# Kernel optimization log

Hardware: AMD Instinct MI355X
Metric: run time of the kernel (lower is better)

The kernel has to match this reference:

```python
import jax, jax.numpy as jnp
import numpy as np

N, E, B = 50000, 300000, 8
XD, ED, H, L, G = 160, 16, 256, 4, 32


def setup_inputs() -> dict:
    key = jax.random.key(0)
    ks = jax.random.split(key, 24)
    w = lambda k, shape: jax.random.normal(k, shape, jnp.float32) * 0.05
    z = lambda *shape: jnp.zeros(shape, jnp.float32)
    in_dim = G + (XD - 128)
    return {
        "x": jax.random.normal(ks[0], (N, XD), jnp.float32),
        "edge_attr": jax.random.normal(ks[1], (E, ED), jnp.float32),
        "geo_w": w(ks[2], (128, G)), "geo_b": z(G),
        "nin_w1": w(ks[3], (in_dim, H)), "nin_b1": z(H),
        "nin_w2": w(ks[4], (H, H)), "nin_b2": z(H),
        "ee_w1": w(ks[5], (ED, H)), "ee_b1": z(H),
        "ee_w2": w(ks[6], (H, H)), "ee_b2": z(H),
        "msgx_w": w(ks[7], (L, H, H)),
        "msge_w": w(ks[8], (L, H, H)),
        "upd_w1": w(ks[9], (L, H, H)), "upd_b1": z(L, H),
        "upd_w2": w(ks[10], (L, H, H)), "upd_b2": z(L, H),
        "ln_g": jnp.ones((L, H), jnp.float32), "ln_b": z(L, H),
        "edge_index": jax.random.randint(ks[11], (2, E), 0, N),
        "batch": jnp.sort(jax.random.randint(ks[12], (N,), 0, B)),
        "node_type": jax.random.randint(ks[13], (N,), 0, 3),
    }


def _layernorm(v, g, b, eps=1e-5):
    mu = v.mean(-1, keepdims=True)
    var = ((v - mu) ** 2).mean(-1, keepdims=True)
    return (v - mu) / jnp.sqrt(var + eps) * g + b


def reference(x, edge_attr, geo_w, geo_b, nin_w1, nin_b1, nin_w2, nin_b2,
              ee_w1, ee_b1, ee_w2, ee_b2, msgx_w, msge_w,
              upd_w1, upd_b1, upd_w2, upd_b2, ln_g, ln_b,
              edge_index, batch, node_type):
    # geo projection of leading 128 dims, concat with remaining features
    geo = jax.nn.relu(x[:, :128] @ geo_w + geo_b)
    xin = jnp.concatenate([geo, x[:, 128:]], axis=1)
    # node_in MLP
    h = jax.nn.relu(xin @ nin_w1 + nin_b1) @ nin_w2 + nin_b2  # [N, H]
    # edge encoder MLP
    e = jax.nn.relu(edge_attr @ ee_w1 + ee_b1) @ ee_w2 + ee_b2  # [E, H]
    src, dst = edge_index[0], edge_index[1]
    for l in range(L):
        # message: msg_x(x_j) + msg_e(e), scatter-add to target nodes
        m = h[src] @ msgx_w[l] + e @ msge_w[l]  # [E, H]
        agg = jax.ops.segment_sum(m, dst, num_segments=N)  # [N, H]
        u = jax.nn.relu(agg @ upd_w1[l] + upd_b1[l]) @ upd_w2[l] + upd_b2[l]
        h = _layernorm(h + u, ln_g[l], ln_b[l])
    # masked mean-pool per graph for each node type
    def pool(k):
        mask = (node_type == k).astype(h.dtype)[:, None]  # [N, 1]
        s = jax.ops.segment_sum(h * mask, batch, num_segments=B)
        c = jax.ops.segment_sum(mask, batch, num_segments=B)
        return s / jnp.maximum(c, 1.0)
    z = jnp.concatenate([pool(0), pool(1), pool(2)], axis=1)  # [B, 3H]
    return (z, h, batch)
```

## Files before the change

kernel.cpp:

```cpp
#include <hip/hip_runtime.h>

constexpr int N  = 50000;
constexpr int E  = 300000;
constexpr int B  = 8;
constexpr int XD = 160;
constexpr int ED = 16;
constexpr int H  = 256;
constexpr int L  = 4;
constexpr int G  = 32;

typedef __attribute__((ext_vector_type(8))) short short8;
typedef __attribute__((ext_vector_type(4))) short sv4;
typedef __attribute__((ext_vector_type(4))) float floatx4;

__device__ __forceinline__ short f2bf(float f) {
    union { float f; unsigned u; } v; v.f = f;
    unsigned r = (v.u + 0x7fffu + ((v.u >> 16) & 1u)) >> 16;
    return (short)r;
}
__device__ __forceinline__ float bf2f(short s) {
    union { unsigned u; float f; } v;
    v.u = ((unsigned)(unsigned short)s) << 16;
    return v.f;
}

__global__ __launch_bounds__(256) void hist_kernel(
    const int* __restrict__ dst, int* __restrict__ cnt)
{
    int e = blockIdx.x * 256 + threadIdx.x;
    if (e < E) atomicAdd(&cnt[dst[e]], 1);
}

__global__ __launch_bounds__(256) void scan_partial_kernel(
    const int* __restrict__ cnt, int* __restrict__ bsum)
{
    __shared__ int s[256];
    const int tid = threadIdx.x;
    int i = blockIdx.x * 256 + tid;
    s[tid] = (i < N) ? cnt[i] : 0;
    __syncthreads();
    #pragma unroll
    for (int off = 128; off > 0; off >>= 1) {
        if (tid < off) s[tid] += s[tid + off];
        __syncthreads();
    }
    if (tid == 0) bsum[blockIdx.x] = s[0];
}

__global__ __launch_bounds__(256) void scan_bsum_kernel(
    int* __restrict__ bsum, int nb, int* __restrict__ rsN)
{
    __shared__ int s[256];
    const int tid = threadIdx.x;
    int v = (tid < nb) ? bsum[tid] : 0;
    s[tid] = v;
    __syncthreads();
    #pragma unroll
    for (int off = 1; off < 256; off <<= 1) {
        int x = (tid >= off) ? s[tid - off] : 0;
        __syncthreads();
        s[tid] += x;
        __syncthreads();
    }
    if (tid < nb) bsum[tid] = s[tid] - v;
    if (tid == 255) *rsN = s[255];
}

__global__ __launch_bounds__(256) void scan_final_kernel(
    const int* __restrict__ cnt, const int* __restrict__ bsum,
    int* __restrict__ rs, int* __restrict__ cursor)
{
    __shared__ int s[256];
    const int tid = threadIdx.x;
    int i = blockIdx.x * 256 + tid;
    int v = (i < N) ? cnt[i] : 0;
    s[tid] = v;
    __syncthreads();
    #pragma unroll
    for (int off = 1; off < 256; off <<= 1) {
        int x = (tid >= off) ? s[tid - off] : 0;
        __syncthreads();
        s[tid] += x;
        __syncthreads();
    }
    int excl = s[tid] - v + bsum[blockIdx.x];
    if (i < N) { rs[i] = excl; cursor[i] = excl; }
}

__global__ __launch_bounds__(256) void fill_kernel(
    const int* __restrict__ src, const int* __restrict__ dst,
    int* __restrict__ cursor, int* __restrict__ csr_src, int* __restrict__ csr_eid)
{
    int e = blockIdx.x * 256 + threadIdx.x;
    if (e < E) {
        int d = dst[e];
        int pos = atomicAdd(&cursor[d], 1);
        csr_src[pos] = src[e];
        csr_eid[pos] = e;
    }
}

__global__ __launch_bounds__(256) void hidden_agg_kernel(
    const float* __restrict__ ea, const float* __restrict__ ew1,
    const float* __restrict__ eb1,
    const int* __restrict__ rs, const int* __restrict__ csr_eid,
    short* __restrict__ haggB)
{
    const int tid = threadIdx.x;
    const int lane = tid & 63, wave = tid >> 6;
    const int n0 = blockIdx.x * 16;

    float4 w[ED];
    #pragma unroll
    for (int k = 0; k < ED; ++k)
        w[k] = *(const float4*)&ew1[k * H + 4 * lane];
    float4 bb = *(const float4*)&eb1[4 * lane];

    #pragma unroll
    for (int t = 0; t < 4; ++t) {
        int n = n0 + wave * 4 + t;
        if (n >= N) continue;
        int s = rs[n], e = rs[n + 1];
        float4 acc = {0.f, 0.f, 0.f, 0.f};
        int j = s;
        for (; j + 1 < e; j += 2) {
            int e0 = csr_eid[j], e1 = csr_eid[j + 1];
            const float* a0 = ea + (size_t)e0 * ED;
            const float* a1 = ea + (size_t)e1 * ED;
            float4 h0 = bb, h1 = bb;
            #pragma unroll
            for (int k = 0; k < ED; ++k) {
                float v0 = a0[k], v1 = a1[k];
                h0.x += v0 * w[k].x; h1.x += v1 * w[k].x;
                h0.y += v0 * w[k].y; h1.y += v1 * w[k].y;
                h0.z += v0 * w[k].z; h1.z += v1 * w[k].z;
                h0.w += v0 * w[k].w; h1.w += v1 * w[k].w;
            }
            acc.x += fmaxf(h0.x, 0.f) + fmaxf(h1.x, 0.f);
            acc.y += fmaxf(h0.y, 0.f) + fmaxf(h1.y, 0.f);
            acc.z += fmaxf(h0.z, 0.f) + fmaxf(h1.z, 0.f);
            acc.w += fmaxf(h0.w, 0.f) + fmaxf(h1.w, 0.f);
        }
        if (j < e) {
            int e0 = csr_eid[j];
            const float* a0 = ea + (size_t)e0 * ED;
            float4 h0 = bb;
            #pragma unroll
            for (int k = 0; k < ED; ++k) {
                float v0 = a0[k];
                h0.x += v0 * w[k].x; h0.y += v0 * w[k].y;
                h0.z += v0 * w[k].z; h0.w += v0 * w[k].w;
            }
            acc.x += fmaxf(h0.x, 0.f); acc.y += fmaxf(h0.y, 0.f);
            acc.z += fmaxf(h0.z, 0.f); acc.w += fmaxf(h0.w, 0.f);
        }
        sv4 o = {f2bf(acc.x), f2bf(acc.y), f2bf(acc.z), f2bf(acc.w)};
        *(sv4*)&haggB[(size_t)n * H + 4 * lane] = o;
    }
}

__global__ __launch_bounds__(256) void gather_kernel(
    const short* __restrict__ h_in_bf,
    const int* __restrict__ rs, const int* __restrict__ csr_src,
    short* __restrict__ agg_bf)
{
    const int lane = threadIdx.x & 63;
    const int wave = threadIdx.x >> 6;
    const int n = blockIdx.x * 4 + wave;
    if (n >= N) return;
    const int s = rs[n], e = rs[n + 1];
    float4 acc = {0.f, 0.f, 0.f, 0.f};
    int j = s;
    for (; j + 4 <= e; j += 4) {
        const int s0 = csr_src[j],     s1 = csr_src[j + 1];
        const int s2 = csr_src[j + 2], s3 = csr_src[j + 3];
        sv4 v0 = *(const sv4*)&h_in_bf[(size_t)s0 * H + 4 * lane];
        sv4 v1 = *(const sv4*)&h_in_bf[(size_t)s1 * H + 4 * lane];
        sv4 v2 = *(const sv4*)&h_in_bf[(size_t)s2 * H + 4 * lane];
        sv4 v3 = *(const sv4*)&h_in_bf[(size_t)s3 * H + 4 * lane];
        acc.x += (bf2f(v0.x) + bf2f(v1.x)) + (bf2f(v2.x) + bf2f(v3.x));
        acc.y += (bf2f(v0.y) + bf2f(v1.y)) + (bf2f(v2.y) + bf2f(v3.y));
        acc.z += (bf2f(v0.z) + bf2f(v1.z)) + (bf2f(v2.z) + bf2f(v3.z));
        acc.w += (bf2f(v0.w) + bf2f(v1.w)) + (bf2f(v2.w) + bf2f(v3.w));
    }
    for (; j < e; ++j) {
        const int s0 = csr_src[j];
        sv4 v0 = *(const sv4*)&h_in_bf[(size_t)s0 * H + 4 * lane];
        acc.x += bf2f(v0.x); acc.y += bf2f(v0.y);
        acc.z += bf2f(v0.z); acc.w += bf2f(v0.w);
    }
    sv4 o = {f2bf(acc.x), f2bf(acc.y), f2bf(acc.z), f2bf(acc.w)};
    *(sv4*)&agg_bf[(size_t)n * H + 4 * lane] = o;
}

__global__ __launch_bounds__(256) void wx_part_kernel(
    const float* __restrict__ msgx_w, short* __restrict__ wxwe)
{
    int l = blockIdx.x >> 8, k = blockIdx.x & 255, n = threadIdx.x;
    wxwe[((size_t)(l * H + n)) * 512 + k] = f2bf(msgx_w[((size_t)l * H + k) * H + n]);
}

__global__ __launch_bounds__(256) void we_fuse_kernel(
    const float* __restrict__ ee_w2, const float* __restrict__ msge_w,
    short* __restrict__ wxwe)
{
    __shared__ float wrow[H];
    const int tid = threadIdx.x;
    const int l = blockIdx.x / H;
    const int t = blockIdx.x % H;
    wrow[tid] = ee_w2[t * H + tid];
    __syncthreads();
    const float* mw = msge_w + (size_t)l * H * H;
    float acc = 0.f;
    for (int k = 0; k < H; ++k)
        acc += wrow[k] * mw[k * H + tid];
    wxwe[((size_t)(l * H + tid)) * 512 + 256 + t] = f2bf(acc);
}

__global__ __launch_bounds__(256) void fuse_b_kernel(
    const float* __restrict__ ee_b2, const float* __restrict__ msge_w,
    float* __restrict__ be2)
{
    __shared__ float brow[H];
    const int tid = threadIdx.x;
    const int l = blockIdx.x;
    brow[tid] = ee_b2[tid];
    __syncthreads();
    const float* mw = msge_w + (size_t)l * H * H;
    float acc = 0.f;
    for (int k = 0; k < H; ++k)
        acc += brow[k] * mw[k * H + tid];
    be2[l * H + tid] = acc;
}

__global__ __launch_bounds__(256) void conv_bt_kernel(
    const float* __restrict__ w, short* __restrict__ bt)
{
    int mat = blockIdx.x >> 8, k = blockIdx.x & 255, n = threadIdx.x;
    bt[((size_t)mat * H + n) * H + k] = f2bf(w[((size_t)mat * H + k) * H + n]);
}

__global__ __launch_bounds__(256) void geow_bt_kernel(
    const float* __restrict__ w, short* __restrict__ bt)
{
    for (int i = threadIdx.x; i < 32 * 128; i += 256) {
        int n = i >> 7, k = i & 127;
        bt[i] = f2bf(w[k * 32 + n]);
    }
}

__global__ __launch_bounds__(256) void ninw1_bt_kernel(
    const float* __restrict__ w, short* __restrict__ bt)
{
    int i = blockIdx.x * 256 + threadIdx.x;
    int n = i >> 6, k = i & 63;
    bt[i] = f2bf(w[k * H + n]);
}

__global__ __launch_bounds__(256) void node_in_mfma_kernel(
    const float* __restrict__ x,
    const short* __restrict__ geo_wbt, const float* __restrict__ geo_b,
    const short* __restrict__ w1bt, const float* __restrict__ b1,
    const short* __restrict__ w2bt, const float* __restrict__ b2,
    short* __restrict__ h_bf)
{
    constexpr int KP = H + 8;
    constexpr int KX = 128 + 8;
    constexpr int KI = 64 + 8;
    __shared__ short A[64 * KP];
    __shared__ short XIN[64 * KI];
    const int tid = threadIdx.x;
    const int lane = tid & 63, wave = tid >> 6;
    const int quad = lane >> 4, lm = lane & 15;
    const int n0 = blockIdx.x * 64;
    const int nvalid = min(64, N - n0);
    const int ncol = wave * 64 + lm;

    for (int i = tid; i < 64 * 128; i += 256) {
        int row = i >> 7, k = i & 127;
        float v = (row < nvalid) ? x[(size_t)(n0 + row) * XD + k] : 0.f;
        A[row * KX + k] = f2bf(v);
    }
    for (int i = tid; i < 64 * 32; i += 256) {
        int row = i >> 5, k = i & 31;
        float v = (row < nvalid) ? x[(size_t)(n0 + row) * XD + 128 + k] : 0.f;
        XIN[row * KI + 32 + k] = f2bf(v);
    }
    __syncthreads();

    {
        floatx4 c[2];
        float b0 = geo_b[lm], b1v = geo_b[16 + lm];
        c[0] = {b0, b0, b0, b0};
        c[1] = {b1v, b1v, b1v, b1v};
        #pragma unroll
        for (int ks = 0; ks < 4; ++ks) {
            short8 a  = *(const short8*)&A[(wave * 16 + lm) * KX + ks * 32 + quad * 8];
            short8 w0 = *(const short8*)&geo_wbt[(size_t)lm * 128 + ks * 32 + quad * 8];
            short8 w1 = *(const short8*)&geo_wbt[(size_t)(16 + lm) * 128 + ks * 32 + quad * 8];
            c[0] = __builtin_amdgcn_mfma_f32_16x16x32_bf16(a, w0, c[0], 0, 0, 0);
            c[1] = __builtin_amdgcn_mfma_f32_16x16x32_bf16(a, w1, c[1], 0, 0, 0);
        }
        #pragma unroll
        for (int nt = 0; nt < 2; ++nt)
            #pragma unroll
            for (int r = 0; r < 4; ++r) {
                int row = wave * 16 + quad * 4 + r;
                XIN[row * KI + nt * 16 + lm] = f2bf(fmaxf(c[nt][r], 0.f));
            }
    }
    __syncthreads();

    floatx4 c1[4][4];
    #pragma unroll
    for (int nt = 0; nt < 4; ++nt) {
        float bb = b1[ncol + nt * 16];
        #pragma unroll
        for (int mt = 0; mt < 4; ++mt) {
            c1[mt][nt][0] = bb; c1[mt][nt][1] = bb;
            c1[mt][nt][2] = bb; c1[mt][nt][3] = bb;
        }
    }
    #pragma unroll
    for (int ks = 0; ks < 2; ++ks) {
        short8 a[4], b[4];
        #pragma unroll
        for (int mt = 0; mt < 4; ++mt)
            a[mt] = *(const short8*)&XIN[(mt * 16 + lm) * KI + ks * 32 + quad * 8];
        #pragma unroll
        for (int nt = 0; nt < 4; ++nt)
            b[nt] = *(const short8*)&w1bt[(size_t)(ncol + nt * 16) * 64 + ks * 32 + quad * 8];
        #pragma unroll
        for (int mt = 0; mt < 4; ++mt)
            #pragma unroll
            for (int nt = 0; nt < 4; ++nt)
                c1[mt][nt] = __builtin_amdgcn_mfma_f32_16x16x32_bf16(a[mt], b[nt], c1[mt][nt], 0, 0, 0);
    }
    __syncthreads();
    #pragma unroll
    for (int mt = 0; mt < 4; ++mt)
        #pragma unroll
        for (int nt = 0; nt < 4; ++nt) {
            int col = ncol + nt * 16;
            #pragma unroll
            for (int r = 0; r < 4; ++r) {
                int row = mt * 16 + quad * 4 + r;
                A[row * KP + col] = f2bf(fmaxf(c1[mt][nt][r], 0.f));
            }
        }
    __syncthreads();

    floatx4 c2[4][4];
    #pragma unroll
    for (int nt = 0; nt < 4; ++nt) {
        float bb = b2[ncol + nt * 16];
        #pragma unroll
        for (int mt = 0; mt < 4; ++mt) {
            c2[mt][nt][0] = bb; c2[mt][nt][1] = bb;
            c2[mt][nt][2] = bb; c2[mt][nt][3] = bb;
        }
    }
    #pragma unroll
    for (int ks = 0; ks < 8; ++ks) {
        short8 a[4], b[4];
        #pragma unroll
        for (int mt = 0; mt < 4; ++mt)
            a[mt] = *(const short8*)&A[(mt * 16 + lm) * KP + ks * 32 + quad * 8];
        #pragma unroll
        for (int nt = 0; nt < 4; ++nt)
            b[nt] = *(const short8*)&w2bt[(size_t)(ncol + nt * 16) * H + ks * 32 + quad * 8];
        #pragma unroll
        for (int mt = 0; mt < 4; ++mt)
            #pragma unroll
            for (int nt = 0; nt < 4; ++nt)
                c2[mt][nt] = __builtin_amdgcn_mfma_f32_16x16x32_bf16(a[mt], b[nt], c2[mt][nt], 0, 0, 0);
    }
    #pragma unroll
    for (int mt = 0; mt < 4; ++mt)
        #pragma unroll
        for (int r = 0; r < 4; ++r) {
            int row = mt * 16 + quad * 4 + r;
            if (row < nvalid) {
                #pragma unroll
                for (int nt = 0; nt < 4; ++nt)
                    h_bf[(size_t)(n0 + row) * H + ncol + nt * 16] = f2bf(c2[mt][nt][r]);
            }
        }
}

__global__ __launch_bounds__(256) void layer_kernel(
    const short* __restrict__ h_in_bf, short* __restrict__ h_out_bf,
    float* __restrict__ h_out_f32,
    const short* __restrict__ agg_bf,
    const int* __restrict__ rs,
    const short* __restrict__ haggB,
    const short* __restrict__ wxwe, const float* __restrict__ be2,
    const short* __restrict__ u1bt, const float* __restrict__ b1,
    const short* __restrict__ u2bt, const float* __restrict__ b2,
    const float* __restrict__ lng, const float* __restrict__ lnb)
{
    constexpr int KP = H + 8;
    constexpr int M  = 32;
    __shared__ short A[M * KP];
    __shared__ int rsL[M + 1];
    __shared__ float psum[M][4], psq[M][4];
    __shared__ float muS[M], rsS[M];
    const int tid  = threadIdx.x;
    const int lane = tid & 63, wave = tid >> 6;
    const int quad = lane >> 4, lm = lane & 15;
    const int n0 = blockIdx.x * M;
    const int nvalid = min(M, N - n0);
    const int ncol = wave * 64 + lm;

    if (tid < M + 1) rsL[tid] = rs[min(n0 + tid, N)];
    for (int i = tid; i < M * 64; i += 256) {
        int row = i >> 6, q = i & 63;
        sv4 v = {0, 0, 0, 0};
        if (row < nvalid)
            v = *(const sv4*)&agg_bf[(size_t)(n0 + row) * H + 4 * q];
        *(sv4*)&A[row * KP + 4 * q] = v;
    }
    __syncthreads();

    floatx4 c1[2][4];
    #pragma unroll
    for (int nt = 0; nt < 4; ++nt) {
        float bb = be2[ncol + nt * 16];
        #pragma unroll
        for (int mt = 0; mt < 2; ++mt) {
            #pragma unroll
            for (int r = 0; r < 4; ++r) {
                int row = mt * 16 + quad * 4 + r;
                float deg = (float)(rsL[row + 1] - rsL[row]);
                c1[mt][nt][r] = deg * bb;
            }
        }
    }
    #pragma unroll
    for (int ks = 0; ks < 8; ++ks) {
        short8 a[2], b[4];
        #pragma unroll
        for (int mt = 0; mt < 2; ++mt)
            a[mt] = *(const short8*)&A[(mt * 16 + lm) * KP + ks * 32 + quad * 8];
        #pragma unroll
        for (int nt = 0; nt < 4; ++nt)
            b[nt] = *(const short8*)&wxwe[(size_t)(ncol + nt * 16) * 512 + ks * 32 + quad * 8];
        #pragma unroll
        for (int mt = 0; mt < 2; ++mt)
            #pragma unroll
            for (int nt = 0; nt < 4; ++nt)
                c1[mt][nt] = __builtin_amdgcn_mfma_f32_16x16x32_bf16(a[mt], b[nt], c1[mt][nt], 0, 0, 0);
    }
    __syncthreads();
    for (int i = tid; i < M * 64; i += 256) {
        int row = i >> 6, q = i & 63;
        sv4 v = {0, 0, 0, 0};
        if (row < nvalid)
            v = *(const sv4*)&haggB[(size_t)(n0 + row) * H + 4 * q];
        *(sv4*)&A[row * KP + 4 * q] = v;
    }
    __syncthreads();
    #pragma unroll
    for (int ks = 0; ks < 8; ++ks) {
        short8 a[2], b[4];
        #pragma unroll
        for (int mt = 0; mt < 2; ++mt)
            a[mt] = *(const short8*)&A[(mt * 16 + lm) * KP + ks * 32 + quad * 8];
        #pragma unroll
        for (int nt = 0; nt < 4; ++nt)
            b[nt] = *(const short8*)&wxwe[(size_t)(ncol + nt * 16) * 512 + 256 + ks * 32 + quad * 8];
        #pragma unroll
        for (int mt = 0; mt < 2; ++mt)
            #pragma unroll
            for (int nt = 0; nt < 4; ++nt)
                c1[mt][nt] = __builtin_amdgcn_mfma_f32_16x16x32_bf16(a[mt], b[nt], c1[mt][nt], 0, 0, 0);
    }
    __syncthreads();
    #pragma unroll
    for (int mt = 0; mt < 2; ++mt)
        #pragma unroll
        for (int nt = 0; nt < 4; ++nt) {
            int col = ncol + nt * 16;
            #pragma unroll
            for (int r = 0; r < 4; ++r) {
                int row = mt * 16 + quad * 4 + r;
                A[row * KP + col] = f2bf(c1[mt][nt][r]);
            }
        }
    __syncthreads();

    floatx4 c2[2][4];
    #pragma unroll
    for (int nt = 0; nt < 4; ++nt) {
        float bb = b1[ncol + nt * 16];
        #pragma unroll
        for (int mt = 0; mt < 2; ++mt) {
            c2[mt][nt][0] = bb; c2[mt][nt][1] = bb;
            c2[mt][nt][2] = bb; c2[mt][nt][3] = bb;
        }
    }
    #pragma unroll
    for (int ks = 0; ks < 8; ++ks) {
        short8 a[2], b[4];
        #pragma unroll
        for (int mt = 0; mt < 2; ++mt)
            a[mt] = *(const short8*)&A[(mt * 16 + lm) * KP + ks * 32 + quad * 8];
        #pragma unroll
        for (int nt = 0; nt < 4; ++nt)
            b[nt] = *(const short8*)&u1bt[(size_t)(ncol + nt * 16) * H + ks * 32 + quad * 8];
        #pragma unroll
        for (int mt = 0; mt < 2; ++mt)
            #pragma unroll
            for (int nt = 0; nt < 4; ++nt)
                c2[mt][nt] = __builtin_amdgcn_mfma_f32_16x16x32_bf16(a[mt], b[nt], c2[mt][nt], 0, 0, 0);
    }
    __syncthreads();
    #pragma unroll
    for (int mt = 0; mt < 2; ++mt)
        #pragma unroll
        for (int nt = 0; nt < 4; ++nt) {
            int col = ncol + nt * 16;
            #pragma unroll
            for (int r = 0; r < 4; ++r) {
                int row = mt * 16 + quad * 4 + r;
                A[row * KP + col] = f2bf(fmaxf(c2[mt][nt][r], 0.f));
            }
        }
    __syncthreads();

    floatx4 c3[2][4];
    #pragma unroll
    for (int nt = 0; nt < 4; ++nt) {
        float bb = b2[ncol + nt * 16];
        #pragma unroll
        for (int mt = 0; mt < 2; ++mt) {
            c3[mt][nt][0] = bb; c3[mt][nt][1] = bb;
            c3[mt][nt][2] = bb; c3[mt][nt][3] = bb;
        }
    }
    #pragma unroll
    for (int ks = 0; ks < 8; ++ks) {
        short8 a[2], b[4];
        #pragma unroll
        for (int mt = 0; mt < 2; ++mt)
            a[mt] = *(const short8*)&A[(mt * 16 + lm) * KP + ks * 32 + quad * 8];
        #pragma unroll
        for (int nt = 0; nt < 4; ++nt)
            b[nt] = *(const short8*)&u2bt[(size_t)(ncol + nt * 16) * H + ks * 32 + quad * 8];
        #pragma unroll
        for (int mt = 0; mt < 2; ++mt)
            #pragma unroll
            for (int nt = 0; nt < 4; ++nt)
                c3[mt][nt] = __builtin_amdgcn_mfma_f32_16x16x32_bf16(a[mt], b[nt], c3[mt][nt], 0, 0, 0);
    }
    #pragma unroll
    for (int mt = 0; mt < 2; ++mt)
        #pragma unroll
        for (int r = 0; r < 4; ++r) {
            int row = mt * 16 + quad * 4 + r;
            if (row < nvalid) {
                #pragma unroll
                for (int nt = 0; nt < 4; ++nt)
                    c3[mt][nt][r] += bf2f(h_in_bf[(size_t)(n0 + row) * H + ncol + nt * 16]);
            }
        }

    #pragma unroll
    for (int mt = 0; mt < 2; ++mt)
        #pragma unroll
        for (int r = 0; r < 4; ++r) {
            float s = 0.f, q = 0.f;
            #pragma unroll
            for (int nt = 0; nt < 4; ++nt) {
                float v = c3[mt][nt][r];
                s += v; q += v * v;
            }
            #pragma unroll
            for (int m = 1; m < 16; m <<= 1) {
                s += __shfl_xor(s, m, 64);
                q += __shfl_xor(q, m, 64);
            }
            if (lm == 0) {
                int row = mt * 16 + quad * 4 + r;
                psum[row][wave] = s;
                psq[row][wave]  = q;
            }
        }
    __syncthreads();
    if (tid < M) {
        float s = psum[tid][0] + psum[tid][1] + psum[tid][2] + psum[tid][3];
        float q = psq[tid][0] + psq[tid][1] + psq[tid][2] + psq[tid][3];
        float mu = s * (1.f / H);
        float var = q * (1.f / H) - mu * mu;
        muS[tid] = mu;
        rsS[tid] = rsqrtf(fmaxf(var, 0.f) + 1e-5f);
    }
    __syncthreads();

    float g[4], bb4[4];
    #pragma unroll
    for (int nt = 0; nt < 4; ++nt) {
        g[nt]   = lng[ncol + nt * 16];
        bb4[nt] = lnb[ncol + nt * 16];
    }
    const bool wbf = (h_out_bf != nullptr);
    const bool wf  = (h_out_f32 != nullptr);
    #pragma unroll
    for (int mt = 0; mt < 2; ++mt)
        #pragma unroll
        for (int r = 0; r < 4; ++r) {
            int row = mt * 16 + quad * 4 + r;
            if (row < nvalid) {
                float mu = muS[row], rsv = rsS[row];
                #pragma unroll
                for (int nt = 0; nt < 4; ++nt) {
                    float o = (c3[mt][nt][r] - mu) * rsv * g[nt] + bb4[nt];
                    size_t off = (size_t)(n0 + row) * H + ncol + nt * 16;
                    if (wbf) h_out_bf[off] = f2bf(o);
                    if (wf)  h_out_f32[off] = o;
                }
            }
        }
}

__global__ __launch_bounds__(256) void pool_kernel(
    const float* __restrict__ h, const int* __restrict__ batch,
    const int* __restrict__ ntype,
    float* __restrict__ zsum, float* __restrict__ zcnt)
{
    constexpr int CHUNK = 256;
    __shared__ float acc[3][H];
    __shared__ float cnt[3];
    const int tid = threadIdx.x;
    const int n0 = blockIdx.x * CHUNK;
    const int nend = min(n0 + CHUNK, N);

    for (int q = 0; q < 3; ++q) acc[q][tid] = 0.f;
    if (tid == 0) { cnt[0] = 0.f; cnt[1] = 0.f; cnt[2] = 0.f; }
    __syncthreads();

    int cur = batch[n0];
    for (int n = n0; n < nend; ++n) {
        int b = batch[n];
        int t = ntype[n];
        if (b != cur) {
            for (int q = 0; q < 3; ++q) {
                atomicAdd(&zsum[cur * (3 * H) + q * H + tid], acc[q][tid]);
                acc[q][tid] = 0.f;
            }
            if (tid == 0)
                for (int q = 0; q < 3; ++q) { atomicAdd(&zcnt[cur * 3 + q], cnt[q]); cnt[q] = 0.f; }
            cur = b;
        }
        acc[t][tid] += h[(size_t)n * H + tid];
        if (tid == 0) cnt[t] += 1.f;
    }
    for (int q = 0; q < 3; ++q)
        atomicAdd(&zsum[cur * (3 * H) + q * H + tid], acc[q][tid]);
    if (tid == 0)
        for (int q = 0; q < 3; ++q) atomicAdd(&zcnt[cur * 3 + q], cnt[q]);
}

__global__ __launch_bounds__(256) void finalize_kernel(
    const float* __restrict__ zsum, const float* __restrict__ zcnt,
    float* __restrict__ out)
{
    int idx = blockIdx.x * 256 + threadIdx.x;
    if (idx >= B * 3 * H) return;
    int b = idx / (3 * H);
    int c = idx % (3 * H);
    int t = c / H;
    float cn = zcnt[b * 3 + t];
    out[idx] = zsum[idx] / fmaxf(cn, 1.f);
}

__global__ __launch_bounds__(256) void batch_out_kernel(
    const int* __restrict__ batch, float* __restrict__ out)
{
    int idx = blockIdx.x * 256 + threadIdx.x;
    if (idx < N) out[idx] = (float)batch[idx];
}

extern "C" void kernel_launch(void* const* d_in, const int* in_sizes, int n_in,
                              void* d_out, int out_size, void* d_ws, size_t ws_size,
                              hipStream_t stream) {
    const float* x         = (const float*)d_in[0];
    const float* edge_attr = (const float*)d_in[1];
    const float* geo_w     = (const float*)d_in[2];
    const float* geo_b     = (const float*)d_in[3];
    const float* nin_w1    = (const float*)d_in[4];
    const float* nin_b1    = (const float*)d_in[5];
    const float* nin_w2    = (const float*)d_in[6];
    const float* nin_b2    = (const float*)d_in[7];
    const float* ee_w1     = (const float*)d_in[8];
    const float* ee_b1     = (const float*)d_in[9];
    const float* ee_w2     = (const float*)d_in[10];
    const float* ee_b2     = (const float*)d_in[11];
    const float* msgx_w    = (const float*)d_in[12];
    const float* msge_w    = (const float*)d_in[13];
    const float* upd_w1    = (const float*)d_in[14];
    const float* upd_b1    = (const float*)d_in[15];
    const float* upd_w2    = (const float*)d_in[16];
    const float* upd_b2    = (const float*)d_in[17];
    const float* ln_g      = (const float*)d_in[18];
    const float* ln_b      = (const float*)d_in[19];
    const int*   edge_index= (const int*)d_in[20];
    const int*   batch     = (const int*)d_in[21];
    const int*   node_type = (const int*)d_in[22];

    float* out = (float*)d_out;
    float* hf  = out + B * 3 * H;

    short* h0_bf   = (short*)d_ws;
    short* h1_bf   = h0_bf + (size_t)N * H;
    short* haggB   = h1_bf + (size_t)N * H;
    short* wxwe    = haggB + (size_t)N * H;
    short* u1bt    = wxwe + (size_t)L * H * 512;
    short* u2bt    = u1bt + (size_t)L * H * H;
    short* geowbt  = u2bt + (size_t)L * H * H;
    short* w1bt    = geowbt + 32 * 128;
    short* w2bt    = w1bt + H * 64;
    float* be2     = (float*)(w2bt + H * H);
    float* zsum    = be2 + L * H;
    float* zcnt    = zsum + B * 3 * H;
    int*   rowcnt  = (int*)(zcnt + B * 3);
    int*   rs      = rowcnt + N;
    int*   cursor  = rs + N + 1;
    int*   bsum    = cursor + N;
    int*   csr_src = bsum + 256;
    int*   csr_eid = csr_src + E;

    const int* src = edge_index;
    const int* dst = edge_index + E;

    const int nscan = (N + 255) / 256;

    hipMemsetAsync(rowcnt, 0, (size_t)N * sizeof(int), stream);
    hist_kernel<<<(E + 255) / 256, 256, 0, stream>>>(dst, rowcnt);
    scan_partial_kernel<<<nscan, 256, 0, stream>>>(rowcnt, bsum);
    scan_bsum_kernel<<<1, 256, 0, stream>>>(bsum, nscan, rs + N);
    scan_final_kernel<<<nscan, 256, 0, stream>>>(rowcnt, bsum, rs, cursor);
    fill_kernel<<<(E + 255) / 256, 256, 0, stream>>>(src, dst, cursor, csr_src, csr_eid);

    wx_part_kernel<<<L * 256, 256, 0, stream>>>(msgx_w, wxwe);
    we_fuse_kernel<<<L * H, 256, 0, stream>>>(ee_w2, msge_w, wxwe);
    fuse_b_kernel<<<L, 256, 0, stream>>>(ee_b2, msge_w, be2);
    conv_bt_kernel<<<L * 256, 256, 0, stream>>>(upd_w1, u1bt);
    conv_bt_kernel<<<L * 256, 256, 0, stream>>>(upd_w2, u2bt);
    conv_bt_kernel<<<256, 256, 0, stream>>>(nin_w2, w2bt);
    geow_bt_kernel<<<1, 256, 0, stream>>>(geo_w, geowbt);
    ninw1_bt_kernel<<<64, 256, 0, stream>>>(nin_w1, w1bt);

    hidden_agg_kernel<<<(N + 15) / 16, 256, 0, stream>>>(
        edge_attr, ee_w1, ee_b1, rs, csr_eid, haggB);

    node_in_mfma_kernel<<<(N + 63) / 64, 256, 0, stream>>>(
        x, geowbt, geo_b, w1bt, nin_b1, w2bt, nin_b2, h0_bf);

    const int lgrid = (N + 31) / 32;
    for (int l = 0; l < L; ++l) {
        const short* hin  = (l & 1) ? h1_bf : h0_bf;
        short* aggb       = (l & 1) ? h0_bf : h1_bf;
        short* hout_bf    = (l == L - 1) ? nullptr : aggb;
        float* hout_f32   = (l == L - 1) ? hf : nullptr;
        gather_kernel<<<(N + 3) / 4, 256, 0, stream>>>(hin, rs, csr_src, aggb);
        layer_kernel<<<lgrid, 256, 0, stream>>>(
            hin, hout_bf, hout_f32, aggb, rs, haggB,
            wxwe + (size_t)l * H * 512, be2 + (size_t)l * H,
            u1bt + (size_t)l * H * H, upd_b1 + (size_t)l * H,
            u2bt + (size_t)l * H * H, upd_b2 + (size_t)l * H,
            ln_g + (size_t)l * H, ln_b + (size_t)l * H);
    }

    hipMemsetAsync(zsum, 0, (size_t)(B * 3 * H + B * 3) * sizeof(float), stream);
    pool_kernel<<<(N + 255) / 256, 256, 0, stream>>>(hf, batch, node_type, zsum, zcnt);
    finalize_kernel<<<(B * 3 * H + 255) / 256, 256, 0, stream>>>(zsum, zcnt, out);
    batch_out_kernel<<<(N + 255) / 256, 256, 0, stream>>>(batch, out + B * 3 * H + (size_t)N * H);
}
```

Baseline: 1.045 ms.

## Split fused layer kernel into message, MLP1 and MLP2+LayerNorm kernels

The single per-layer kernel, which staged activations through a padded LDS tile across three chained GEMMs, is replaced by three kernels. They pass intermediates through a new global bf16 buffer and read MFMA A-operands straight from global memory. Dropping the LDS tile and the many block barriers, and adding a launch bound of four blocks per CU, aims to raise occupancy and remove synchronisation stalls. The cost is extra global writes and reads of an N×H intermediate per layer, plus two more launches per layer. The last partial tile also reads rows past N, which only lands in adjacent workspace.

```diff
diff --git a/kernel.cpp b/kernel.cpp
--- a/kernel.cpp
+++ b/kernel.cpp
@@ -388,21 +388,141 @@
         }
 }
 
-__global__ __launch_bounds__(256) void layer_kernel(
+
+__global__ __launch_bounds__(256, 4) void msg_kernel(
+    const short* __restrict__ agg_bf, const short* __restrict__ haggB,
+    const int* __restrict__ rs,
+    const short* __restrict__ wxwe, const float* __restrict__ be2,
+    short* __restrict__ m_bf)
+{
+    constexpr int M = 32;
+    __shared__ int rsL[M + 1];
+    const int tid  = threadIdx.x;
+    const int lane = tid & 63, wave = tid >> 6;
+    const int quad = lane >> 4, lm = lane & 15;
+    const int n0 = blockIdx.x * M;
+    const int nvalid = min(M, N - n0);
+    const int ncol = wave * 64 + lm;
+
+    if (tid < M + 1) rsL[tid] = rs[min(n0 + tid, N)];
+    __syncthreads();
+
+    floatx4 c[2][4];
+    #pragma unroll
+    for (int nt = 0; nt < 4; ++nt) {
+        float bb = be2[ncol + nt * 16];
+        #pragma unroll
+        for (int mt = 0; mt < 2; ++mt) {
+            #pragma unroll
+            for (int r = 0; r < 4; ++r) {
+                int row = mt * 16 + quad * 4 + r;
+                float deg = (float)(rsL[row + 1] - rsL[row]);
+                c[mt][nt][r] = deg * bb;
+            }
+        }
+    }
+    #pragma unroll
+    for (int ks = 0; ks < 8; ++ks) {
+        short8 a[2], b[4];
+        #pragma unroll
+        for (int mt = 0; mt < 2; ++mt)
+            a[mt] = *(const short8*)&agg_bf[(size_t)(n0 + mt * 16 + lm) * H + ks * 32 + quad * 8];
+        #pragma unroll
+        for (int nt = 0; nt < 4; ++nt)
+            b[nt] = *(const short8*)&wxwe[(size_t)(ncol + nt * 16) * 512 + ks * 32 + quad * 8];
+        #pragma unroll
+        for (int mt = 0; mt < 2; ++mt)
+            #pragma unroll
+            for (int nt = 0; nt < 4; ++nt)
+                c[mt][nt] = __builtin_amdgcn_mfma_f32_16x16x32_bf16(a[mt], b[nt], c[mt][nt], 0, 0, 0);
+    }
+    #pragma unroll
+    for (int ks = 0; ks < 8; ++ks) {
+        short8 a[2], b[4];
+        #pragma unroll
+        for (int mt = 0; mt < 2; ++mt)
+            a[mt] = *(const short8*)&haggB[(size_t)(n0 + mt * 16 + lm) * H + ks * 32 + quad * 8];
+        #pragma unroll
+        for (int nt = 0; nt < 4; ++nt)
+            b[nt] = *(const short8*)&wxwe[(size_t)(ncol + nt * 16) * 512 + 256 + ks * 32 + quad * 8];
+        #pragma unroll
+        for (int mt = 0; mt < 2; ++mt)
+            #pragma unroll
+            for (int nt = 0; nt < 4; ++nt)
+                c[mt][nt] = __builtin_amdgcn_mfma_f32_16x16x32_bf16(a[mt], b[nt], c[mt][nt], 0, 0, 0);
+    }
+    #pragma unroll
+    for (int mt = 0; mt < 2; ++mt)
+        #pragma unroll
+        for (int r = 0; r < 4; ++r) {
+            int row = mt * 16 + quad * 4 + r;
+            if (row < nvalid) {
+                #pragma unroll
+                for (int nt = 0; nt < 4; ++nt)
+                    m_bf[(size_t)(n0 + row) * H + ncol + nt * 16] = f2bf(c[mt][nt][r]);
+            }
+        }
+}
+
+__global__ __launch_bounds__(256, 4) void mlp1_kernel(
+    short* __restrict__ m_bf,
+    const short* __restrict__ u1bt, const float* __restrict__ b1)
+{
+    constexpr int M = 32;
+    const int tid  = threadIdx.x;
+    const int lane = tid & 63, wave = tid >> 6;
+    const int quad = lane >> 4, lm = lane & 15;
+    const int n0 = blockIdx.x * M;
+    const int nvalid = min(M, N - n0);
+    const int ncol = wave * 64 + lm;
+
+    floatx4 c[2][4];
+    #pragma unroll
+    for (int nt = 0; nt < 4; ++nt) {
+        float bb = b1[ncol + nt * 16];
+        #pragma unroll
+        for (int mt = 0; mt < 2; ++mt) {
+            c[mt][nt][0] = bb; c[mt][nt][1] = bb;
+            c[mt][nt][2] = bb; c[mt][nt][3] = bb;
+        }
+    }
+    #pragma unroll
+    for (int ks = 0; ks < 8; ++ks) {
+        short8 a[2], b[4];
+        #pragma unroll
+        for (int mt = 0; mt < 2; ++mt)
+            a[mt] = *(const short8*)&m_bf[(size_t)(n0 + mt * 16 + lm) * H + ks * 32 + quad * 8];
+        #pragma unroll
+        for (int nt = 0; nt < 4; ++nt)
+            b[nt] = *(const short8*)&u1bt[(size_t)(ncol + nt * 16) * H + ks * 32 + quad * 8];
+        #pragma unroll
+        for (int mt = 0; mt < 2; ++mt)
+            #pragma unroll
+            for (int nt = 0; nt < 4; ++nt)
+                c[mt][nt] = __builtin_amdgcn_mfma_f32_16x16x32_bf16(a[mt], b[nt], c[mt][nt], 0, 0, 0);
+    }
+    __syncthreads();
+    #pragma unroll
+    for (int mt = 0; mt < 2; ++mt)
+        #pragma unroll
+        for (int r = 0; r < 4; ++r) {
+            int row = mt * 16 + quad * 4 + r;
+            if (row < nvalid) {
+                #pragma unroll
+                for (int nt = 0; nt < 4; ++nt)
+                    m_bf[(size_t)(n0 + row) * H + ncol + nt * 16] = f2bf(fmaxf(c[mt][nt][r], 0.f));
+            }
+        }
+}
+
+__global__ __launch_bounds__(256, 4) void mlp2_ln_kernel(
     const short* __restrict__ h_in_bf, short* __restrict__ h_out_bf,
     float* __restrict__ h_out_f32,
-    const short* __restrict__ agg_bf,
-    const int* __restrict__ rs,
-    const short* __restrict__ haggB,
-    const short* __restrict__ wxwe, const float* __restrict__ be2,
-    const short* __restrict__ u1bt, const float* __restrict__ b1,
+    const short* __restrict__ u_bf,
     const short* __restrict__ u2bt, const float* __restrict__ b2,
     const float* __restrict__ lng, const float* __restrict__ lnb)
 {
-    constexpr int KP = H + 8;
-    constexpr int M  = 32;
-    __shared__ short A[M * KP];
-    __shared__ int rsL[M + 1];
+    constexpr int M = 32;
     __shared__ float psum[M][4], psq[M][4];
     __shared__ float muS[M], rsS[M];
     const int tid  = threadIdx.x;
@@ -412,28 +532,14 @@
     const int nvalid = min(M, N - n0);
     const int ncol = wave * 64 + lm;
 
-    if (tid < M + 1) rsL[tid] = rs[min(n0 + tid, N)];
-    for (int i = tid; i < M * 64; i += 256) {
-        int row = i >> 6, q = i & 63;
-        sv4 v = {0, 0, 0, 0};
-        if (row < nvalid)
-            v = *(const sv4*)&agg_bf[(size_t)(n0 + row) * H + 4 * q];
-        *(sv4*)&A[row * KP + 4 * q] = v;
-    }
-    __syncthreads();
-
-    floatx4 c1[2][4];
+    floatx4 c[2][4];
     #pragma unroll
     for (int nt = 0; nt < 4; ++nt) {
-        float bb = be2[ncol + nt * 16];
+        float bb = b2[ncol + nt * 16];
         #pragma unroll
         for (int mt = 0; mt < 2; ++mt) {
-            #pragma unroll
-            for (int r = 0; r < 4; ++r) {
-                int row = mt * 16 + quad * 4 + r;
-                float deg = (float)(rsL[row + 1] - rsL[row]);
-                c1[mt][nt][r] = deg * bb;
-            }
+            c[mt][nt][0] = bb; c[mt][nt][1] = bb;
+            c[mt][nt][2] = bb; c[mt][nt][3] = bb;
         }
     }
     #pragma unroll
@@ -441,109 +547,7 @@
         short8 a[2], b[4];
         #pragma unroll
         for (int mt = 0; mt < 2; ++mt)
-            a[mt] = *(const short8*)&A[(mt * 16 + lm) * KP + ks * 32 + quad * 8];
-        #pragma unroll
-        for (int nt = 0; nt < 4; ++nt)
-            b[nt] = *(const short8*)&wxwe[(size_t)(ncol + nt * 16) * 512 + ks * 32 + quad * 8];
-        #pragma unroll
-        for (int mt = 0; mt < 2; ++mt)
-            #pragma unroll
-            for (int nt = 0; nt < 4; ++nt)
-                c1[mt][nt] = __builtin_amdgcn_mfma_f32_16x16x32_bf16(a[mt], b[nt], c1[mt][nt], 0, 0, 0);
-    }
-    __syncthreads();
-    for (int i = tid; i < M * 64; i += 256) {
-        int row = i >> 6, q = i & 63;
-        sv4 v = {0, 0, 0, 0};
-        if (row < nvalid)
-            v = *(const sv4*)&haggB[(size_t)(n0 + row) * H + 4 * q];
-        *(sv4*)&A[row * KP + 4 * q] = v;
-    }
-    __syncthreads();
-    #pragma unroll
-    for (int ks = 0; ks < 8; ++ks) {
-        short8 a[2], b[4];
-        #pragma unroll
-        for (int mt = 0; mt < 2; ++mt)
-            a[mt] = *(const short8*)&A[(mt * 16 + lm) * KP + ks * 32 + quad * 8];
-        #pragma unroll
-        for (int nt = 0; nt < 4; ++nt)
-            b[nt] = *(const short8*)&wxwe[(size_t)(ncol + nt * 16) * 512 + 256 + ks * 32 + quad * 8];
-        #pragma unroll
-        for (int mt = 0; mt < 2; ++mt)
-            #pragma unroll
-            for (int nt = 0; nt < 4; ++nt)
-                c1[mt][nt] = __builtin_amdgcn_mfma_f32_16x16x32_bf16(a[mt], b[nt], c1[mt][nt], 0, 0, 0);
-    }
-    __syncthreads();
-    #pragma unroll
-    for (int mt = 0; mt < 2; ++mt)
-        #pragma unroll
-        for (int nt = 0; nt < 4; ++nt) {
-            int col = ncol + nt * 16;
-            #pragma unroll
-            for (int r = 0; r < 4; ++r) {
-                int row = mt * 16 + quad * 4 + r;
-                A[row * KP + col] = f2bf(c1[mt][nt][r]);
-            }
-        }
-    __syncthreads();
-
-    floatx4 c2[2][4];
-    #pragma unroll
-    for (int nt = 0; nt < 4; ++nt) {
-        float bb = b1[ncol + nt * 16];
-        #pragma unroll
-        for (int mt = 0; mt < 2; ++mt) {
-            c2[mt][nt][0] = bb; c2[mt][nt][1] = bb;
-            c2[mt][nt][2] = bb; c2[mt][nt][3] = bb;
-        }
-    }
-    #pragma unroll
-    for (int ks = 0; ks < 8; ++ks) {
-        short8 a[2], b[4];
-        #pragma unroll
-        for (int mt = 0; mt < 2; ++mt)
-            a[mt] = *(const short8*)&A[(mt * 16 + lm) * KP + ks * 32 + quad * 8];
-        #pragma unroll
-        for (int nt = 0; nt < 4; ++nt)
-            b[nt] = *(const short8*)&u1bt[(size_t)(ncol + nt * 16) * H + ks * 32 + quad * 8];
-        #pragma unroll
-        for (int mt = 0; mt < 2; ++mt)
-            #pragma unroll
-            for (int nt = 0; nt < 4; ++nt)
-                c2[mt][nt] = __builtin_amdgcn_mfma_f32_16x16x32_bf16(a[mt], b[nt], c2[mt][nt], 0, 0, 0);
-    }
-    __syncthreads();
-    #pragma unroll
-    for (int mt = 0; mt < 2; ++mt)
-        #pragma unroll
-        for (int nt = 0; nt < 4; ++nt) {
-            int col = ncol + nt * 16;
-            #pragma unroll
-            for (int r = 0; r < 4; ++r) {
-                int row = mt * 16 + quad * 4 + r;
-                A[row * KP + col] = f2bf(fmaxf(c2[mt][nt][r], 0.f));
-            }
-        }
-    __syncthreads();
-
-    floatx4 c3[2][4];
-    #pragma unroll
-    for (int nt = 0; nt < 4; ++nt) {
-        float bb = b2[ncol + nt * 16];
-        #pragma unroll
-        for (int mt = 0; mt < 2; ++mt) {
-            c3[mt][nt][0] = bb; c3[mt][nt][1] = bb;
-            c3[mt][nt][2] = bb; c3[mt][nt][3] = bb;
-        }
-    }
-    #pragma unroll
-    for (int ks = 0; ks < 8; ++ks) {
-        short8 a[2], b[4];
-        #pragma unroll
-        for (int mt = 0; mt < 2; ++mt)
-            a[mt] = *(const short8*)&A[(mt * 16 + lm) * KP + ks * 32 + quad * 8];
+            a[mt] = *(const short8*)&u_bf[(size_t)(n0 + mt * 16 + lm) * H + ks * 32 + quad * 8];
         #pragma unroll
         for (int nt = 0; nt < 4; ++nt)
             b[nt] = *(const short8*)&u2bt[(size_t)(ncol + nt * 16) * H + ks * 32 + quad * 8];
@@ -551,7 +555,7 @@
         for (int mt = 0; mt < 2; ++mt)
             #pragma unroll
             for (int nt = 0; nt < 4; ++nt)
-                c3[mt][nt] = __builtin_amdgcn_mfma_f32_16x16x32_bf16(a[mt], b[nt], c3[mt][nt], 0, 0, 0);
+                c[mt][nt] = __builtin_amdgcn_mfma_f32_16x16x32_bf16(a[mt], b[nt], c[mt][nt], 0, 0, 0);
     }
     #pragma unroll
     for (int mt = 0; mt < 2; ++mt)
@@ -561,7 +565,7 @@
             if (row < nvalid) {
                 #pragma unroll
                 for (int nt = 0; nt < 4; ++nt)
-                    c3[mt][nt][r] += bf2f(h_in_bf[(size_t)(n0 + row) * H + ncol + nt * 16]);
+                    c[mt][nt][r] += bf2f(h_in_bf[(size_t)(n0 + row) * H + ncol + nt * 16]);
             }
         }
 
@@ -572,7 +576,7 @@
             float s = 0.f, q = 0.f;
             #pragma unroll
             for (int nt = 0; nt < 4; ++nt) {
-                float v = c3[mt][nt][r];
+                float v = c[mt][nt][r];
                 s += v; q += v * v;
             }
             #pragma unroll
@@ -614,7 +618,7 @@
                 float mu = muS[row], rsv = rsS[row];
                 #pragma unroll
                 for (int nt = 0; nt < 4; ++nt) {
-                    float o = (c3[mt][nt][r] - mu) * rsv * g[nt] + bb4[nt];
+                    float o = (c[mt][nt][r] - mu) * rsv * g[nt] + bb4[nt];
                     size_t off = (size_t)(n0 + row) * H + ncol + nt * 16;
                     if (wbf) h_out_bf[off] = f2bf(o);
                     if (wf)  h_out_f32[off] = o;
@@ -714,7 +718,8 @@
     short* h0_bf   = (short*)d_ws;
     short* h1_bf   = h0_bf + (size_t)N * H;
     short* haggB   = h1_bf + (size_t)N * H;
-    short* wxwe    = haggB + (size_t)N * H;
+    short* m_bf    = haggB + (size_t)N * H;
+    short* wxwe    = m_bf + (size_t)N * H;
     short* u1bt    = wxwe + (size_t)L * H * 512;
     short* u2bt    = u1bt + (size_t)L * H * H;
     short* geowbt  = u2bt + (size_t)L * H * H;
@@ -764,10 +769,12 @@
         short* hout_bf    = (l == L - 1) ? nullptr : aggb;
         float* hout_f32   = (l == L - 1) ? hf : nullptr;
         gather_kernel<<<(N + 3) / 4, 256, 0, stream>>>(hin, rs, csr_src, aggb);
-        layer_kernel<<<lgrid, 256, 0, stream>>>(
-            hin, hout_bf, hout_f32, aggb, rs, haggB,
-            wxwe + (size_t)l * H * 512, be2 + (size_t)l * H,
-            u1bt + (size_t)l * H * H, upd_b1 + (size_t)l * H,
+        msg_kernel<<<lgrid, 256, 0, stream>>>(
+            aggb, haggB, rs, wxwe + (size_t)l * H * 512, be2 + (size_t)l * H, m_bf);
+        mlp1_kernel<<<lgrid, 256, 0, stream>>>(
+            m_bf, u1bt + (size_t)l * H * H, upd_b1 + (size_t)l * H);
+        mlp2_ln_kernel<<<lgrid, 256, 0, stream>>>(
+            hin, hout_bf, hout_f32, m_bf,
             u2bt + (size_t)l * H * H, upd_b2 + (size_t)l * H,
             ln_g + (size_t)l * H, ln_b + (size_t)l * H);
     }
```

Result: slower. 1.255 ms (+20.1%).
